# Kernel tuning notes

Hardware: AMD Instinct MI355X
Metric: run time of the kernel (lower is better)

The kernel has to match this reference:

```python
import jax, jax.numpy as jnp
import numpy as np

D_MODEL = 1024  # scale uses sqrt(d_model), matching the source's sqrt(C)

def setup_inputs() -> dict:
    key = jax.random.key(0)
    kx, kq, kk, kv = jax.random.split(key, 4)
    B, T, C, H = 8, 2048, D_MODEL, 64
    s = 1.0 / np.sqrt(C)
    return {
        "x": jax.random.normal(kx, (B, T, C), dtype=jnp.float32),
        "Wq": jax.random.normal(kq, (C, H), dtype=jnp.float32) * s,
        "Wk": jax.random.normal(kk, (C, H), dtype=jnp.float32) * s,
        "Wv": jax.random.normal(kv, (C, H), dtype=jnp.float32) * s,
    }

def reference(x, Wq, Wk, Wv):
    B, T, C = x.shape
    q = jnp.einsum("btc,ch->bth", x, Wq)
    k = jnp.einsum("btc,ch->bth", x, Wk)
    v = jnp.einsum("btc,ch->bth", x, Wv)
    # scores scaled by 1/sqrt(C) (C = d_model), faithful to source
    wei = jnp.einsum("bth,bsh->bts", q, k) / jnp.sqrt(jnp.float32(C))
    causal = jnp.tril(jnp.ones((T, T), dtype=bool))  # [T, T]
    wei = jnp.where(causal, wei, -jnp.inf)
    wei = jax.nn.softmax(wei, axis=-1)
    out = jnp.einsum("bts,bsh->bth", wei, v)
    return out
```

## Files before the change

### kernel.cpp

```cpp
#include <hip/hip_runtime.h>

typedef unsigned short u16;
typedef __attribute__((ext_vector_type(4))) float f32x4;
typedef __attribute__((ext_vector_type(8))) short bf16x8;
typedef __attribute__((ext_vector_type(4))) u16 u16x4;

#define MFMA(a, b, c) __builtin_amdgcn_mfma_f32_16x16x32_bf16(a, b, c, 0, 0, 0)

__device__ __forceinline__ u16 f2bf(float f) {
    unsigned u = __float_as_uint(f);
    u += 0x7fffu + ((u >> 16) & 1u);
    return (u16)(u >> 16);
}
__device__ __forceinline__ float bf2f(u16 h) {
    unsigned u = ((unsigned)h) << 16;
    return __uint_as_float(u);
}

__device__ __forceinline__ void load_lds16(const void* g, void* l) {
    __builtin_amdgcn_global_load_lds((const __attribute__((address_space(1))) void*)g,
                                     (__attribute__((address_space(3))) void*)l,
                                     16, 0, 0);
}

__global__ void wt_pack(const float* __restrict__ Wq, const float* __restrict__ Wk,
                        const float* __restrict__ Wv, u16* __restrict__ Wtt) {
    const int k = blockIdx.x;
    const int n = threadIdx.x;
    const float* W = (n < 64) ? Wq : (n < 128 ? Wk : Wv);
    const float v = W[(size_t)k * 64 + (n & 63)];
    const int kt = k >> 6, ks = k & 63, c = ks >> 3, ci = ks & 7;
    Wtt[(size_t)kt * 12288 + n * 64 + (((c ^ (n & 7)) << 3) + ci)] = f2bf(v);
}

__global__ __launch_bounds__(256, 2) void qkv_gemm(const float* __restrict__ x,
                                                   const u16* __restrict__ Wtt,
                                                   u16* __restrict__ qo,
                                                   u16* __restrict__ ko,
                                                   u16* __restrict__ vT) {
    const int tid = threadIdx.x;
    const int lane = tid & 63, wave = tid >> 6;
    const int lr = lane & 15, lg = lane >> 4;
    const int m0 = blockIdx.x * 32;

    __shared__ __align__(16) float xs[2][32 * 64];
    __shared__ __align__(16) u16 ws[2][192 * 64];

    f32x4 acc[2][3];
#pragma unroll
    for (int m = 0; m < 2; ++m)
#pragma unroll
        for (int n = 0; n < 3; ++n) acc[m][n] = (f32x4){0.f, 0.f, 0.f, 0.f};

    const int srow = tid >> 4;
    const int schk = tid & 15;

    {
#pragma unroll
        for (int j = 0; j < 2; ++j) {
            const int rr = j * 16 + srow;
            const float* src = x + (size_t)(m0 + rr) * 1024 + ((schk ^ (rr & 7)) << 2);
            load_lds16(src, &xs[0][j * 1024 + wave * 256]);
        }
#pragma unroll
        for (int j = 0; j < 6; ++j) {
            const u16* src = Wtt + (size_t)j * 2048 + tid * 8;
            load_lds16(src, &ws[0][j * 2048 + wave * 512]);
        }
    }
    __syncthreads();

    for (int kt = 0; kt < 16; ++kt) {
        const int cur = kt & 1;
        if (kt < 15) {
            const int nxt = cur ^ 1;
#pragma unroll
            for (int j = 0; j < 2; ++j) {
                const int rr = j * 16 + srow;
                const float* src =
                    x + (size_t)(m0 + rr) * 1024 + (kt + 1) * 64 + ((schk ^ (rr & 7)) << 2);
                load_lds16(src, &xs[nxt][j * 1024 + wave * 256]);
            }
#pragma unroll
            for (int j = 0; j < 6; ++j) {
                const u16* src = Wtt + (size_t)(kt + 1) * 12288 + j * 2048 + tid * 8;
                load_lds16(src, &ws[nxt][j * 2048 + wave * 512]);
            }
        }
#pragma unroll
        for (int h = 0; h < 2; ++h) {
            bf16x8 a[2];
#pragma unroll
            for (int mm = 0; mm < 2; ++mm) {
                const int rr = mm * 16 + lr;
                const int c0 = h * 8 + lg * 2;
                f32x4 f0 = *(const f32x4*)&xs[cur][rr * 64 + ((c0 ^ (rr & 7)) << 2)];
                f32x4 f1 = *(const f32x4*)&xs[cur][rr * 64 + (((c0 + 1) ^ (rr & 7)) << 2)];
                bf16x8 t;
#pragma unroll
                for (int i = 0; i < 4; ++i) {
                    t[i] = (short)f2bf(f0[i]);
                    t[i + 4] = (short)f2bf(f1[i]);
                }
                a[mm] = t;
            }
#pragma unroll
            for (int nl = 0; nl < 3; ++nl) {
                const int row = (wave * 3 + nl) * 16 + lr;
                const int cb = h * 4 + lg;
                const bf16x8 b = *(const bf16x8*)&ws[cur][row * 64 + ((cb ^ (row & 7)) << 3)];
                acc[0][nl] = MFMA(a[0], b, acc[0][nl]);
                acc[1][nl] = MFMA(a[1], b, acc[1][nl]);
            }
        }
        __syncthreads();
    }

    const float SCQ = 0.0450842200277801f;
    const int bb = m0 >> 11;
    const int tb = m0 & 2047;
#pragma unroll
    for (int mm = 0; mm < 2; ++mm)
#pragma unroll
        for (int nl = 0; nl < 3; ++nl) {
            const int col = (wave * 3 + nl) * 16 + lr;
            const int rl = mm * 16 + lg * 4;
            if (col < 64) {
#pragma unroll
                for (int r = 0; r < 4; ++r)
                    qo[(size_t)(m0 + rl + r) * 64 + col] = f2bf(acc[mm][nl][r] * SCQ);
            } else if (col < 128) {
#pragma unroll
                for (int r = 0; r < 4; ++r)
                    ko[(size_t)(m0 + rl + r) * 64 + (col - 64)] = f2bf(acc[mm][nl][r]);
            } else {
                u16x4 pk;
#pragma unroll
                for (int r = 0; r < 4; ++r) pk[r] = f2bf(acc[mm][nl][r]);
                *(u16x4*)&vT[(size_t)(bb * 64 + (col - 128)) * 2048 + tb + rl] = pk;
            }
        }
}

#define PPITCH 72
__global__ __launch_bounds__(256, 2) void attn_part(const u16* __restrict__ q,
                                                    const u16* __restrict__ k,
                                                    const u16* __restrict__ vT,
                                                    u16* __restrict__ Opb,
                                                    float* __restrict__ Lp) {
    const int b = blockIdx.x & 7;
    int g = blockIdx.x >> 3;
    int qt = 31, rem = g;
    while (rem >= (qt >> 3) + 1) { rem -= (qt >> 3) + 1; --qt; }
    const int c0 = rem;
    const int q0 = qt * 64;
    const int kv_lo = c0 * 512;
    const int kv_hi = min(kv_lo + 512, q0 + 64);
    const int niter = (kv_hi - kv_lo) >> 6;
    const int slot = (b * 32 + qt) * 4 + c0;

    __shared__ __align__(16) u16 lK[3][64 * 64];
    __shared__ __align__(16) u16 lV[3][64 * 64];
    __shared__ __align__(16) u16 lP[4][16 * PPITCH];

    const int tid = threadIdx.x;
    const int wave = tid >> 6, lane = tid & 63;
    const int lr = lane & 15, lg = lane >> 4;

    const u16* qb = q + (size_t)b * 2048 * 64;
    const u16* kb = k + (size_t)b * 2048 * 64;
    const u16* vb = vT + (size_t)b * 64 * 2048;

    const int myrow = q0 + wave * 16 + lr;
    const bf16x8 qf0 = *(const bf16x8*)(qb + (size_t)myrow * 64 + lg * 8);
    const bf16x8 qf1 = *(const bf16x8*)(qb + (size_t)myrow * 64 + 32 + lg * 8);

    f32x4 oacc[4];
#pragma unroll
    for (int n = 0; n < 4; ++n) oacc[n] = (f32x4){0.f, 0.f, 0.f, 0.f};
    float rs = 0.f;

#define ASTAGE(bufi, kv0_)                                                             \
    {                                                                                  \
        _Pragma("unroll") for (int j = 0; j < 2; ++j) {                                \
            const int cid = j * 256 + wave * 64 + lane;                                \
            const int row = cid >> 3, cc = cid & 7;                                    \
            load_lds16(kb + (size_t)((kv0_) + row) * 64 + ((cc ^ (row & 7)) << 3),     \
                       &lK[bufi][(j * 256 + wave * 64) * 8]);                          \
            load_lds16(vb + (size_t)row * 2048 + (kv0_) + ((cc ^ (row & 7)) << 3),     \
                       &lV[bufi][(j * 256 + wave * 64) * 8]);                          \
        }                                                                              \
    }

    ASTAGE(0, kv_lo);
    if (niter > 1) {
        ASTAGE(1, kv_lo + 64);
        asm volatile("s_waitcnt vmcnt(4)" ::: "memory");
    } else {
        asm volatile("s_waitcnt vmcnt(0)" ::: "memory");
    }
    __builtin_amdgcn_s_barrier();
    __builtin_amdgcn_sched_barrier(0);

    for (int it = 0; it < niter; ++it) {
        const int cur = it % 3;
        const int kv0 = kv_lo + it * 64;

        if (kv0 <= q0 + wave * 16 + 15) {
            f32x4 s[4];
#pragma unroll
            for (int n = 0; n < 4; ++n) {
                const int row = n * 16 + lr;
                const bf16x8 kf0 = *(const bf16x8*)&lK[cur][row * 64 + ((lg ^ (row & 7)) << 3)];
                const bf16x8 kf1 =
                    *(const bf16x8*)&lK[cur][row * 64 + (((4 + lg) ^ (row & 7)) << 3)];
                f32x4 a = (f32x4){0.f, 0.f, 0.f, 0.f};
                a = MFMA(kf0, qf0, a);
                a = MFMA(kf1, qf1, a);
                s[n] = a;
            }

            const bool msk = (kv0 + 63 > q0 + wave * 16);
#pragma unroll
            for (int n = 0; n < 4; ++n) {
                u16x4 pk;
#pragma unroll
                for (int r = 0; r < 4; ++r) {
                    const int kvi = kv0 + n * 16 + lg * 4 + r;
                    const float p = (!msk || kvi <= myrow) ? exp2f(s[n][r]) : 0.f;
                    rs += p;
                    pk[r] = f2bf(p);
                }
                *(u16x4*)&lP[wave][lr * PPITCH + n * 16 + lg * 4] = pk;
            }

#pragma unroll
            for (int kc = 0; kc < 2; ++kc) {
                const bf16x8 pf = *(const bf16x8*)&lP[wave][lr * PPITCH + kc * 32 + lg * 8];
#pragma unroll
                for (int n = 0; n < 4; ++n) {
                    const int row = n * 16 + lr;
                    const bf16x8 vf =
                        *(const bf16x8*)&lV[cur][row * 64 + (((kc * 4 + lg) ^ (row & 7)) << 3)];
                    oacc[n] = MFMA(pf, vf, oacc[n]);
                }
            }
        }

        if (it + 2 < niter) ASTAGE((it + 2) % 3, kv_lo + (it + 2) * 64);

        if (it + 1 < niter) {
            if (it + 2 < niter) {
                asm volatile("s_waitcnt vmcnt(4)" ::: "memory");
            } else {
                asm volatile("s_waitcnt vmcnt(0)" ::: "memory");
            }
            __builtin_amdgcn_s_barrier();
            __builtin_amdgcn_sched_barrier(0);
        }
    }

    rs += __shfl_xor(rs, 16);
    rs += __shfl_xor(rs, 32);
    if (lane < 16) Lp[slot * 64 + wave * 16 + lr] = rs;

    u16* op = Opb + (size_t)slot * 4096 + wave * 1024;
#pragma unroll
    for (int n = 0; n < 4; ++n)
#pragma unroll
        for (int r = 0; r < 4; ++r)
            op[n * 256 + (lg * 4 + r) * 16 + lr] = f2bf(oacc[n][r]);
}

__global__ __launch_bounds__(256) void attn_combine(const u16* __restrict__ Opb,
                                                    const float* __restrict__ Lp,
                                                    float* __restrict__ out) {
    const int gid = blockIdx.x * 256 + threadIdx.x;
    const int col = gid & 63;
    const int row = gid >> 6;
    const int b = row >> 11, tt = row & 2047;
    const int qt = tt >> 6, i = tt & 63;
    const int nc = (qt >> 3) + 1;
    const size_t sbase = (size_t)(b * 32 + qt) * 4;
    const int sub = (i >> 4) * 1024 + (col >> 4) * 256 + (i & 15) * 16 + (col & 15);

    float O = 0.f, L = 0.f;
    for (int c = 0; c < nc; ++c) {
        O += bf2f(Opb[(sbase + c) * 4096 + sub]);
        L += Lp[(sbase + c) * 64 + i];
    }
    out[(size_t)row * 64 + col] = O / L;
}

extern "C" void kernel_launch(void* const* d_in, const int* in_sizes, int n_in,
                              void* d_out, int out_size, void* d_ws, size_t ws_size,
                              hipStream_t stream) {
    const float* x = (const float*)d_in[0];
    const float* Wq = (const float*)d_in[1];
    const float* Wk = (const float*)d_in[2];
    const float* Wv = (const float*)d_in[3];
    float* out = (float*)d_out;

    char* ws = (char*)d_ws;
    u16* Wtt = (u16*)ws;
    u16* qb = (u16*)(ws + (512 << 10));
    u16* kb = (u16*)(ws + (512 << 10) + (2 << 20));
    u16* vT = (u16*)(ws + (512 << 10) + (4 << 20));
    u16* Opb = (u16*)(ws + (8 << 20));
    float* Lp = (float*)(ws + (20 << 20));

    wt_pack<<<1024, 192, 0, stream>>>(Wq, Wk, Wv, Wtt);
    qkv_gemm<<<512, 256, 0, stream>>>(x, Wtt, qb, kb, vT);
    attn_part<<<640, 256, 0, stream>>>(qb, kb, vT, Opb, Lp);
    attn_combine<<<4096, 256, 0, stream>>>(Opb, Lp, out);
}
```

Measured before the change: 60.94 us.

## Fuse split-KV combine into attention via last-block atomic counter; double-buffer KV

Removes the separate combine kernel. Each attention block increments a per-(batch, q-tile) counter, and the last block to arrive sums the partial outputs and row sums and writes the normalized result. The counters are zeroed in the weight-pack kernel. The KV pipeline also drops from triple to double buffering with plain __syncthreads, and launch bounds are raised to 3 blocks per CU to improve occupancy. This saves one launch and a pass over the partials, but adds serialized tail work in the last block and less prefetch depth.

```diff
diff --git a/kernel.cpp b/kernel.cpp
--- a/kernel.cpp
+++ b/kernel.cpp
@@ -24,7 +24,9 @@
 }
 
 __global__ void wt_pack(const float* __restrict__ Wq, const float* __restrict__ Wk,
-                        const float* __restrict__ Wv, u16* __restrict__ Wtt) {
+                        const float* __restrict__ Wv, u16* __restrict__ Wtt,
+                        int* __restrict__ cnt) {
+    if (threadIdx.x == 0 && blockIdx.x < 256) cnt[blockIdx.x] = 0;
     const int k = blockIdx.x;
     const int n = threadIdx.x;
     const float* W = (n < 64) ? Wq : (n < 128 ? Wk : Wv);
@@ -143,11 +145,13 @@
 }
 
 #define PPITCH 72
-__global__ __launch_bounds__(256, 2) void attn_part(const u16* __restrict__ q,
+__global__ __launch_bounds__(256, 3) void attn_part(const u16* __restrict__ q,
                                                     const u16* __restrict__ k,
                                                     const u16* __restrict__ vT,
                                                     u16* __restrict__ Opb,
-                                                    float* __restrict__ Lp) {
+                                                    float* __restrict__ Lp,
+                                                    int* __restrict__ cnt,
+                                                    float* __restrict__ out) {
     const int b = blockIdx.x & 7;
     int g = blockIdx.x >> 3;
     int qt = 31, rem = g;
@@ -156,12 +160,15 @@
     const int q0 = qt * 64;
     const int kv_lo = c0 * 512;
     const int kv_hi = min(kv_lo + 512, q0 + 64);
-    const int niter = (kv_hi - kv_lo) >> 6;
+    const int ntiles = (kv_hi - kv_lo) >> 6;
+    const int nc = (qt >> 3) + 1;
     const int slot = (b * 32 + qt) * 4 + c0;
 
-    __shared__ __align__(16) u16 lK[3][64 * 64];
-    __shared__ __align__(16) u16 lV[3][64 * 64];
+    __shared__ __align__(16) u16 lK[2][64 * 64];
+    __shared__ __align__(16) u16 lV[2][64 * 64];
     __shared__ __align__(16) u16 lP[4][16 * PPITCH];
+    __shared__ float Ls[64];
+    __shared__ int lastflag;
 
     const int tid = threadIdx.x;
     const int wave = tid >> 6, lane = tid & 63;
@@ -193,19 +200,13 @@
     }
 
     ASTAGE(0, kv_lo);
-    if (niter > 1) {
-        ASTAGE(1, kv_lo + 64);
-        asm volatile("s_waitcnt vmcnt(4)" ::: "memory");
-    } else {
-        asm volatile("s_waitcnt vmcnt(0)" ::: "memory");
-    }
-    __builtin_amdgcn_s_barrier();
-    __builtin_amdgcn_sched_barrier(0);
-
-    for (int it = 0; it < niter; ++it) {
-        const int cur = it % 3;
+    __syncthreads();
+
+    for (int it = 0; it < ntiles; ++it) {
+        const int cur = it & 1;
+        if (it + 1 < ntiles) ASTAGE(cur ^ 1, kv_lo + (it + 1) * 64);
+
         const int kv0 = kv_lo + it * 64;
-
         if (kv0 <= q0 + wave * 16 + 15) {
             f32x4 s[4];
 #pragma unroll
@@ -246,18 +247,7 @@
                 }
             }
         }
-
-        if (it + 2 < niter) ASTAGE((it + 2) % 3, kv_lo + (it + 2) * 64);
-
-        if (it + 1 < niter) {
-            if (it + 2 < niter) {
-                asm volatile("s_waitcnt vmcnt(4)" ::: "memory");
-            } else {
-                asm volatile("s_waitcnt vmcnt(0)" ::: "memory");
-            }
-            __builtin_amdgcn_s_barrier();
-            __builtin_amdgcn_sched_barrier(0);
-        }
+        __syncthreads();
     }
 
     rs += __shfl_xor(rs, 16);
@@ -270,26 +260,35 @@
 #pragma unroll
         for (int r = 0; r < 4; ++r)
             op[n * 256 + (lg * 4 + r) * 16 + lr] = f2bf(oacc[n][r]);
-}
-
-__global__ __launch_bounds__(256) void attn_combine(const u16* __restrict__ Opb,
-                                                    const float* __restrict__ Lp,
-                                                    float* __restrict__ out) {
-    const int gid = blockIdx.x * 256 + threadIdx.x;
-    const int col = gid & 63;
-    const int row = gid >> 6;
-    const int b = row >> 11, tt = row & 2047;
-    const int qt = tt >> 6, i = tt & 63;
-    const int nc = (qt >> 3) + 1;
-    const size_t sbase = (size_t)(b * 32 + qt) * 4;
-    const int sub = (i >> 4) * 1024 + (col >> 4) * 256 + (i & 15) * 16 + (col & 15);
-
-    float O = 0.f, L = 0.f;
-    for (int c = 0; c < nc; ++c) {
-        O += bf2f(Opb[(sbase + c) * 4096 + sub]);
-        L += Lp[(sbase + c) * 64 + i];
-    }
-    out[(size_t)row * 64 + col] = O / L;
+
+    __threadfence();
+    __syncthreads();
+    if (tid == 0) {
+        const int old = atomicAdd(&cnt[b * 32 + qt], 1);
+        lastflag = (old == nc - 1);
+    }
+    __syncthreads();
+    if (!lastflag) return;
+    __threadfence();
+
+    const size_t sb = (size_t)(b * 32 + qt) * 4;
+    if (tid < 64) {
+        float L = 0.f;
+        for (int c = 0; c < nc; ++c) L += Lp[(sb + c) * 64 + tid];
+        Ls[tid] = 1.0f / L;
+    }
+    __syncthreads();
+
+    float* ob = out + ((size_t)b * 2048 + q0) * 64;
+#pragma unroll
+    for (int j = 0; j < 16; ++j) {
+        const int sub = j * 256 + tid;
+        float O = 0.f;
+        for (int c = 0; c < nc; ++c) O += bf2f(Opb[(sb + c) * 4096 + sub]);
+        const int i = ((sub >> 10) << 4) + ((sub >> 4) & 15);
+        const int col = (((sub >> 8) & 3) << 4) + (sub & 15);
+        ob[i * 64 + col] = O * Ls[i];
+    }
 }
 
 extern "C" void kernel_launch(void* const* d_in, const int* in_sizes, int n_in,
@@ -308,9 +307,9 @@
     u16* vT = (u16*)(ws + (512 << 10) + (4 << 20));
     u16* Opb = (u16*)(ws + (8 << 20));
     float* Lp = (float*)(ws + (20 << 20));
-
-    wt_pack<<<1024, 192, 0, stream>>>(Wq, Wk, Wv, Wtt);
+    int* cnt = (int*)(ws + (21 << 20));
+
+    wt_pack<<<1024, 192, 0, stream>>>(Wq, Wk, Wv, Wtt, cnt);
     qkv_gemm<<<512, 256, 0, stream>>>(x, Wtt, qb, kb, vT);
-    attn_part<<<640, 256, 0, stream>>>(qb, kb, vT, Opb, Lp);
-    attn_combine<<<4096, 256, 0, stream>>>(Opb, Lp, out);
-}
+    attn_part<<<640, 256, 0, stream>>>(qb, kb, vT, Opb, Lp, cnt, out);
+}
```

Measured after the change: 158.3 us. 160% more time.

## Use 128-row query tiles per block so each K/V tile serves two row groups

Applied to the files above, without the earlier changes.

Each attention block now handles 128 query rows instead of 64, with each wave owning two 16-row groups. Every K/V tile staged into LDS is therefore reused twice, halving K/V global traffic per query row and halving the grid size. The LDS pipeline drops from a triple buffer with vmcnt waits to a double buffer with __syncthreads. Occupancy is raised to 3 blocks per SM. The trade-off is fewer blocks (320) for load balancing, more registers per wave, and less overlap of loads with compute.

```diff
diff --git a/kernel.cpp b/kernel.cpp
--- a/kernel.cpp
+++ b/kernel.cpp
@@ -143,24 +143,24 @@
 }
 
 #define PPITCH 72
-__global__ __launch_bounds__(256, 2) void attn_part(const u16* __restrict__ q,
+__global__ __launch_bounds__(256, 3) void attn_part(const u16* __restrict__ q,
                                                     const u16* __restrict__ k,
                                                     const u16* __restrict__ vT,
                                                     u16* __restrict__ Opb,
                                                     float* __restrict__ Lp) {
     const int b = blockIdx.x & 7;
     int g = blockIdx.x >> 3;
-    int qt = 31, rem = g;
-    while (rem >= (qt >> 3) + 1) { rem -= (qt >> 3) + 1; --qt; }
+    int qt = 15, rem = g;
+    while (rem >= (qt >> 2) + 1) { rem -= (qt >> 2) + 1; --qt; }
     const int c0 = rem;
-    const int q0 = qt * 64;
+    const int q0 = qt * 128;
     const int kv_lo = c0 * 512;
-    const int kv_hi = min(kv_lo + 512, q0 + 64);
-    const int niter = (kv_hi - kv_lo) >> 6;
-    const int slot = (b * 32 + qt) * 4 + c0;
-
-    __shared__ __align__(16) u16 lK[3][64 * 64];
-    __shared__ __align__(16) u16 lV[3][64 * 64];
+    const int kv_hi = min(kv_lo + 512, q0 + 128);
+    const int ntiles = (kv_hi - kv_lo) >> 6;
+    const int slot = (b * 16 + qt) * 4 + c0;
+
+    __shared__ __align__(16) u16 lK[2][64 * 64];
+    __shared__ __align__(16) u16 lV[2][64 * 64];
     __shared__ __align__(16) u16 lP[4][16 * PPITCH];
 
     const int tid = threadIdx.x;
@@ -171,14 +171,21 @@
     const u16* kb = k + (size_t)b * 2048 * 64;
     const u16* vb = vT + (size_t)b * 64 * 2048;
 
-    const int myrow = q0 + wave * 16 + lr;
-    const bf16x8 qf0 = *(const bf16x8*)(qb + (size_t)myrow * 64 + lg * 8);
-    const bf16x8 qf1 = *(const bf16x8*)(qb + (size_t)myrow * 64 + 32 + lg * 8);
-
-    f32x4 oacc[4];
-#pragma unroll
-    for (int n = 0; n < 4; ++n) oacc[n] = (f32x4){0.f, 0.f, 0.f, 0.f};
-    float rs = 0.f;
+    const int rbase = q0 + wave * 32;
+    bf16x8 qf[2][2];
+#pragma unroll
+    for (int h = 0; h < 2; ++h) {
+        const u16* qp = qb + (size_t)(rbase + h * 16 + lr) * 64 + lg * 8;
+        qf[h][0] = *(const bf16x8*)(qp);
+        qf[h][1] = *(const bf16x8*)(qp + 32);
+    }
+
+    f32x4 oacc[2][4];
+#pragma unroll
+    for (int h = 0; h < 2; ++h)
+#pragma unroll
+        for (int n = 0; n < 4; ++n) oacc[h][n] = (f32x4){0.f, 0.f, 0.f, 0.f};
+    float rs[2] = {0.f, 0.f};
 
 #define ASTAGE(bufi, kv0_)                                                             \
     {                                                                                  \
@@ -193,83 +200,79 @@
     }
 
     ASTAGE(0, kv_lo);
-    if (niter > 1) {
-        ASTAGE(1, kv_lo + 64);
-        asm volatile("s_waitcnt vmcnt(4)" ::: "memory");
-    } else {
-        asm volatile("s_waitcnt vmcnt(0)" ::: "memory");
-    }
-    __builtin_amdgcn_s_barrier();
-    __builtin_amdgcn_sched_barrier(0);
-
-    for (int it = 0; it < niter; ++it) {
-        const int cur = it % 3;
+    __syncthreads();
+
+    for (int it = 0; it < ntiles; ++it) {
+        const int cur = it & 1;
+        if (it + 1 < ntiles) ASTAGE(cur ^ 1, kv_lo + (it + 1) * 64);
+
         const int kv0 = kv_lo + it * 64;
-
-        if (kv0 <= q0 + wave * 16 + 15) {
-            f32x4 s[4];
-#pragma unroll
-            for (int n = 0; n < 4; ++n) {
-                const int row = n * 16 + lr;
-                const bf16x8 kf0 = *(const bf16x8*)&lK[cur][row * 64 + ((lg ^ (row & 7)) << 3)];
-                const bf16x8 kf1 =
-                    *(const bf16x8*)&lK[cur][row * 64 + (((4 + lg) ^ (row & 7)) << 3)];
-                f32x4 a = (f32x4){0.f, 0.f, 0.f, 0.f};
-                a = MFMA(kf0, qf0, a);
-                a = MFMA(kf1, qf1, a);
-                s[n] = a;
-            }
-
-            const bool msk = (kv0 + 63 > q0 + wave * 16);
-#pragma unroll
-            for (int n = 0; n < 4; ++n) {
-                u16x4 pk;
-#pragma unroll
-                for (int r = 0; r < 4; ++r) {
-                    const int kvi = kv0 + n * 16 + lg * 4 + r;
-                    const float p = (!msk || kvi <= myrow) ? exp2f(s[n][r]) : 0.f;
-                    rs += p;
-                    pk[r] = f2bf(p);
-                }
-                *(u16x4*)&lP[wave][lr * PPITCH + n * 16 + lg * 4] = pk;
-            }
-
-#pragma unroll
-            for (int kc = 0; kc < 2; ++kc) {
-                const bf16x8 pf = *(const bf16x8*)&lP[wave][lr * PPITCH + kc * 32 + lg * 8];
+#pragma unroll
+        for (int h = 0; h < 2; ++h) {
+            const int sb = rbase + h * 16;
+            if (kv0 <= sb + 15) {
+                f32x4 s[4];
 #pragma unroll
                 for (int n = 0; n < 4; ++n) {
                     const int row = n * 16 + lr;
-                    const bf16x8 vf =
-                        *(const bf16x8*)&lV[cur][row * 64 + (((kc * 4 + lg) ^ (row & 7)) << 3)];
-                    oacc[n] = MFMA(pf, vf, oacc[n]);
+                    const bf16x8 kf0 =
+                        *(const bf16x8*)&lK[cur][row * 64 + ((lg ^ (row & 7)) << 3)];
+                    const bf16x8 kf1 =
+                        *(const bf16x8*)&lK[cur][row * 64 + (((4 + lg) ^ (row & 7)) << 3)];
+                    f32x4 a = (f32x4){0.f, 0.f, 0.f, 0.f};
+                    a = MFMA(kf0, qf[h][0], a);
+                    a = MFMA(kf1, qf[h][1], a);
+                    s[n] = a;
                 }
-            }
-        }
-
-        if (it + 2 < niter) ASTAGE((it + 2) % 3, kv_lo + (it + 2) * 64);
-
-        if (it + 1 < niter) {
-            if (it + 2 < niter) {
-                asm volatile("s_waitcnt vmcnt(4)" ::: "memory");
-            } else {
-                asm volatile("s_waitcnt vmcnt(0)" ::: "memory");
-            }
-            __builtin_amdgcn_s_barrier();
-            __builtin_amdgcn_sched_barrier(0);
-        }
-    }
-
-    rs += __shfl_xor(rs, 16);
-    rs += __shfl_xor(rs, 32);
-    if (lane < 16) Lp[slot * 64 + wave * 16 + lr] = rs;
-
-    u16* op = Opb + (size_t)slot * 4096 + wave * 1024;
-#pragma unroll
-    for (int n = 0; n < 4; ++n)
-#pragma unroll
-        for (int r = 0; r < 4; ++r)
-            op[n * 256 + (lg * 4 + r) * 16 + lr] = f2bf(oacc[n][r]);
+
+                const bool msk = (kv0 + 63 > sb);
+                const int myrow = sb + lr;
+#pragma unroll
+                for (int n = 0; n < 4; ++n) {
+                    u16x4 pk;
+#pragma unroll
+                    for (int r = 0; r < 4; ++r) {
+                        const int kvi = kv0 + n * 16 + lg * 4 + r;
+                        const float p = (!msk || kvi <= myrow) ? exp2f(s[n][r]) : 0.f;
+                        rs[h] += p;
+                        pk[r] = f2bf(p);
+                    }
+                    *(u16x4*)&lP[wave][lr * PPITCH + n * 16 + lg * 4] = pk;
+                }
+
+#pragma unroll
+                for (int kc = 0; kc < 2; ++kc) {
+                    const bf16x8 pf =
+                        *(const bf16x8*)&lP[wave][lr * PPITCH + kc * 32 + lg * 8];
+#pragma unroll
+                    for (int n = 0; n < 4; ++n) {
+                        const int row = n * 16 + lr;
+                        const bf16x8 vf = *(const bf16x8*)&lV[cur][row * 64 +
+                                                                   (((kc * 4 + lg) ^ (row & 7))
+                                                                    << 3)];
+                        oacc[h][n] = MFMA(pf, vf, oacc[h][n]);
+                    }
+                }
+            }
+        }
+        __syncthreads();
+    }
+
+#pragma unroll
+    for (int h = 0; h < 2; ++h) {
+        rs[h] += __shfl_xor(rs[h], 16);
+        rs[h] += __shfl_xor(rs[h], 32);
+        if (lane < 16) Lp[slot * 128 + wave * 32 + h * 16 + lr] = rs[h];
+    }
+
+    u16* op = Opb + (size_t)slot * 8192 + wave * 2048;
+#pragma unroll
+    for (int h = 0; h < 2; ++h)
+#pragma unroll
+        for (int n = 0; n < 4; ++n)
+#pragma unroll
+            for (int r = 0; r < 4; ++r)
+                op[h * 1024 + n * 256 + (lg * 4 + r) * 16 + lr] = f2bf(oacc[h][n][r]);
 }
 
 __global__ __launch_bounds__(256) void attn_combine(const u16* __restrict__ Opb,
@@ -279,15 +282,16 @@
     const int col = gid & 63;
     const int row = gid >> 6;
     const int b = row >> 11, tt = row & 2047;
-    const int qt = tt >> 6, i = tt & 63;
-    const int nc = (qt >> 3) + 1;
-    const size_t sbase = (size_t)(b * 32 + qt) * 4;
-    const int sub = (i >> 4) * 1024 + (col >> 4) * 256 + (i & 15) * 16 + (col & 15);
+    const int qt = tt >> 7, i = tt & 127;
+    const int nc = (qt >> 2) + 1;
+    const size_t sbase = (size_t)(b * 16 + qt) * 4;
+    const int sub = (i >> 5) * 2048 + ((i >> 4) & 1) * 1024 + (col >> 4) * 256 +
+                    (i & 15) * 16 + (col & 15);
 
     float O = 0.f, L = 0.f;
     for (int c = 0; c < nc; ++c) {
-        O += bf2f(Opb[(sbase + c) * 4096 + sub]);
-        L += Lp[(sbase + c) * 64 + i];
+        O += bf2f(Opb[(sbase + c) * 8192 + sub]);
+        L += Lp[(sbase + c) * 128 + i];
     }
     out[(size_t)row * 64 + col] = O / L;
 }
@@ -311,6 +315,6 @@
 
     wt_pack<<<1024, 192, 0, stream>>>(Wq, Wk, Wv, Wtt);
     qkv_gemm<<<512, 256, 0, stream>>>(x, Wtt, qb, kb, vT);
-    attn_part<<<640, 256, 0, stream>>>(qb, kb, vT, Opb, Lp);
+    attn_part<<<320, 256, 0, stream>>>(qb, kb, vT, Opb, Lp);
     attn_combine<<<4096, 256, 0, stream>>>(Opb, Lp, out);
 }
```

New measurement: 61.16 us. No clear change (+0.4%).

## Switch attention to double-buffered LDS with 3 waves/EU and vectorize combine

Applied to the files above, without the earlier changes.

The attention kernel goes from a triple-buffered K/V pipeline with explicit vmcnt waits to a simpler double buffer. The next tile is prefetched at the top of each iteration and __syncthreads runs at the end. The smaller LDS footprint and launch_bounds of 3 aim to raise occupancy, at the cost of a shallower prefetch and a full vmcnt(0) wait at every barrier. The combine kernel now has each thread handle 8 contiguous columns with 16-byte loads, vector stores and one reciprocal, cutting its grid by 8x to reduce per-element overhead.

```diff
diff --git a/kernel.cpp b/kernel.cpp
--- a/kernel.cpp
+++ b/kernel.cpp
@@ -4,6 +4,7 @@
 typedef __attribute__((ext_vector_type(4))) float f32x4;
 typedef __attribute__((ext_vector_type(8))) short bf16x8;
 typedef __attribute__((ext_vector_type(4))) u16 u16x4;
+typedef __attribute__((ext_vector_type(8))) u16 u16x8;
 
 #define MFMA(a, b, c) __builtin_amdgcn_mfma_f32_16x16x32_bf16(a, b, c, 0, 0, 0)
 
@@ -143,7 +144,7 @@
 }
 
 #define PPITCH 72
-__global__ __launch_bounds__(256, 2) void attn_part(const u16* __restrict__ q,
+__global__ __launch_bounds__(256, 3) void attn_part(const u16* __restrict__ q,
                                                     const u16* __restrict__ k,
                                                     const u16* __restrict__ vT,
                                                     u16* __restrict__ Opb,
@@ -156,11 +157,11 @@
     const int q0 = qt * 64;
     const int kv_lo = c0 * 512;
     const int kv_hi = min(kv_lo + 512, q0 + 64);
-    const int niter = (kv_hi - kv_lo) >> 6;
+    const int ntiles = (kv_hi - kv_lo) >> 6;
     const int slot = (b * 32 + qt) * 4 + c0;
 
-    __shared__ __align__(16) u16 lK[3][64 * 64];
-    __shared__ __align__(16) u16 lV[3][64 * 64];
+    __shared__ __align__(16) u16 lK[2][64 * 64];
+    __shared__ __align__(16) u16 lV[2][64 * 64];
     __shared__ __align__(16) u16 lP[4][16 * PPITCH];
 
     const int tid = threadIdx.x;
@@ -193,19 +194,13 @@
     }
 
     ASTAGE(0, kv_lo);
-    if (niter > 1) {
-        ASTAGE(1, kv_lo + 64);
-        asm volatile("s_waitcnt vmcnt(4)" ::: "memory");
-    } else {
-        asm volatile("s_waitcnt vmcnt(0)" ::: "memory");
-    }
-    __builtin_amdgcn_s_barrier();
-    __builtin_amdgcn_sched_barrier(0);
-
-    for (int it = 0; it < niter; ++it) {
-        const int cur = it % 3;
+    __syncthreads();
+
+    for (int it = 0; it < ntiles; ++it) {
+        const int cur = it & 1;
+        if (it + 1 < ntiles) ASTAGE(cur ^ 1, kv_lo + (it + 1) * 64);
+
         const int kv0 = kv_lo + it * 64;
-
         if (kv0 <= q0 + wave * 16 + 15) {
             f32x4 s[4];
 #pragma unroll
@@ -246,18 +241,7 @@
                 }
             }
         }
-
-        if (it + 2 < niter) ASTAGE((it + 2) % 3, kv_lo + (it + 2) * 64);
-
-        if (it + 1 < niter) {
-            if (it + 2 < niter) {
-                asm volatile("s_waitcnt vmcnt(4)" ::: "memory");
-            } else {
-                asm volatile("s_waitcnt vmcnt(0)" ::: "memory");
-            }
-            __builtin_amdgcn_s_barrier();
-            __builtin_amdgcn_sched_barrier(0);
-        }
+        __syncthreads();
     }
 
     rs += __shfl_xor(rs, 16);
@@ -276,20 +260,32 @@
                                                     const float* __restrict__ Lp,
                                                     float* __restrict__ out) {
     const int gid = blockIdx.x * 256 + threadIdx.x;
-    const int col = gid & 63;
-    const int row = gid >> 6;
+    const int colg = gid & 7;
+    const int row = gid >> 3;
     const int b = row >> 11, tt = row & 2047;
     const int qt = tt >> 6, i = tt & 63;
     const int nc = (qt >> 3) + 1;
     const size_t sbase = (size_t)(b * 32 + qt) * 4;
-    const int sub = (i >> 4) * 1024 + (col >> 4) * 256 + (i & 15) * 16 + (col & 15);
-
-    float O = 0.f, L = 0.f;
+    const int sub0 = (i >> 4) * 1024 + (colg >> 1) * 256 + (i & 15) * 16 + (colg & 1) * 8;
+
+    float O[8] = {0.f, 0.f, 0.f, 0.f, 0.f, 0.f, 0.f, 0.f};
+    float L = 0.f;
     for (int c = 0; c < nc; ++c) {
-        O += bf2f(Opb[(sbase + c) * 4096 + sub]);
+        const u16x8 v = *(const u16x8*)&Opb[(sbase + c) * 4096 + sub0];
+#pragma unroll
+        for (int j = 0; j < 8; ++j) O[j] += bf2f(v[j]);
         L += Lp[(sbase + c) * 64 + i];
     }
-    out[(size_t)row * 64 + col] = O / L;
+    const float rinv = 1.0f / L;
+    f32x4 o0, o1;
+#pragma unroll
+    for (int j = 0; j < 4; ++j) {
+        o0[j] = O[j] * rinv;
+        o1[j] = O[4 + j] * rinv;
+    }
+    float* ob = out + (size_t)row * 64 + colg * 8;
+    *(f32x4*)(ob) = o0;
+    *(f32x4*)(ob + 4) = o1;
 }
 
 extern "C" void kernel_launch(void* const* d_in, const int* in_sizes, int n_in,
@@ -312,5 +308,5 @@
     wt_pack<<<1024, 192, 0, stream>>>(Wq, Wk, Wv, Wtt);
     qkv_gemm<<<512, 256, 0, stream>>>(x, Wtt, qb, kb, vT);
     attn_part<<<640, 256, 0, stream>>>(qb, kb, vT, Opb, Lp);
-    attn_combine<<<4096, 256, 0, stream>>>(Opb, Lp, out);
-}
+    attn_combine<<<512, 256, 0, stream>>>(Opb, Lp, out);
+}
```

After: 54.99 us. 9.8% less time.
